# Kernel optimization log

Measured on AMD Instinct MI355X. Metric: run time of the kernel, lower is better.

The kernel has to match this reference:

```python
import jax, jax.numpy as jnp
import numpy as np

B, S, D, H = 2, 2048, 1024, 16
HD = D // H
EPS = 1e-5

def _ln(x, g, b):
    mu = jnp.mean(x, axis=-1, keepdims=True)
    var = jnp.var(x, axis=-1, keepdims=True)
    return (x - mu) * jax.lax.rsqrt(var + EPS) * g + b

def setup_inputs() -> dict:
    key = jax.random.key(0)
    ks = jax.random.split(key, 6)
    sc = lambda n: 1.0 / np.sqrt(n)
    return {
        "x": jax.random.normal(ks[0], (B, S, D), jnp.float32),
        "W_qkv": jax.random.normal(ks[1], (D, 3 * D), jnp.float32) * sc(D),
        "b_qkv": jnp.zeros((3 * D,), jnp.float32),
        "W_o": jax.random.normal(ks[2], (D, D), jnp.float32) * sc(D),
        "b_o": jnp.zeros((D,), jnp.float32),
        "W_fc": jax.random.normal(ks[3], (D, 4 * D), jnp.float32) * sc(D),
        "b_fc": jnp.zeros((4 * D,), jnp.float32),
        "W_pr": jax.random.normal(ks[4], (4 * D, D), jnp.float32) * sc(4 * D),
        "b_pr": jnp.zeros((D,), jnp.float32),
        "g1": jnp.ones((D,), jnp.float32),
        "beta1": jnp.zeros((D,), jnp.float32),
        "g2": jnp.ones((D,), jnp.float32),
        "beta2": jnp.zeros((D,), jnp.float32),
    }

def reference(x, W_qkv, b_qkv, W_o, b_o, W_fc, b_fc, W_pr, b_pr, g1, beta1, g2, beta2):
    # pre-norm attention
    h = _ln(x, g1, beta1)
    qkv = h @ W_qkv + b_qkv                      # [B,S,3D]
    q, k, v = jnp.split(qkv, 3, axis=-1)
    q = q.reshape(B, S, H, HD).transpose(0, 2, 1, 3)  # [B,H,S,hd]
    k = k.reshape(B, S, H, HD).transpose(0, 2, 1, 3)
    v = v.reshape(B, S, H, HD).transpose(0, 2, 1, 3)
    scores = jnp.einsum('bhqd,bhkd->bhqk', q, k) / np.sqrt(HD)
    causal = jnp.tril(jnp.ones((S, S), bool))
    scores = jnp.where(causal, scores, -jnp.inf)
    attn = jax.nn.softmax(scores, axis=-1)
    out = jnp.einsum('bhqk,bhkd->bhqd', attn, v)
    out = out.transpose(0, 2, 1, 3).reshape(B, S, D)
    x = x + out @ W_o + b_o
    # pre-norm MLP (exact erf GELU, matching torch F.gelu default)
    h2 = _ln(x, g2, beta2)
    h2 = jax.nn.gelu(h2 @ W_fc + b_fc, approximate=False)
    x = x + h2 @ W_pr + b_pr
    return x
```

## Files before the change

kernel.cpp:

```cpp
#include <hip/hip_runtime.h>
#include <cstdint>
#include <cstddef>

#define Bb 2
#define Ss 2048
#define Dd 1024
#define Hh 16

typedef __attribute__((ext_vector_type(8))) short short8;
typedef __attribute__((ext_vector_type(4))) short short4v;
typedef __attribute__((ext_vector_type(4))) float float4v;

__device__ inline short f2bf(float f) {
  unsigned u = __builtin_bit_cast(unsigned, f);
  u = (u + 0x7fffu + ((u >> 16) & 1u)) >> 16;
  return (short)u;
}

__device__ inline float bf2f(short s) {
  unsigned u = ((unsigned)(unsigned short)s) << 16;
  return __builtin_bit_cast(float, u);
}

__device__ inline void gl_lds16(const void* g, void* l) {
  __builtin_amdgcn_global_load_lds(
      (__attribute__((address_space(1))) void*)(void*)(g),
      (__attribute__((address_space(3))) void*)(l), 16, 0, 0);
}

#define MFMA(a, b, c) __builtin_amdgcn_mfma_f32_16x16x32_bf16((a), (b), (c), 0, 0, 0)

__device__ __forceinline__ void ln_row(const float* __restrict__ x,
                                       const float* __restrict__ g,
                                       const float* __restrict__ be,
                                       short* __restrict__ out, int row,
                                       float* red) {
  int tid = threadIdx.x;
  const float4* xr = (const float4*)(x + (size_t)row * Dd);
  float4 v = xr[tid];
  float s = v.x + v.y + v.z + v.w;
  float q = v.x * v.x + v.y * v.y + v.z * v.z + v.w * v.w;
#pragma unroll
  for (int off = 1; off < 64; off <<= 1) {
    s += __shfl_xor(s, off);
    q += __shfl_xor(q, off);
  }
  int w = tid >> 6;
  if ((tid & 63) == 0) { red[w] = s; red[4 + w] = q; }
  __syncthreads();
  s = red[0] + red[1] + red[2] + red[3];
  q = red[4] + red[5] + red[6] + red[7];
  float mu = s * (1.0f / Dd);
  float var = q * (1.0f / Dd) - mu * mu;
  float rstd = rsqrtf(var + 1e-5f);
  float4 gv = ((const float4*)g)[tid], bv = ((const float4*)be)[tid];
  short4v o;
  o.x = f2bf((v.x - mu) * rstd * gv.x + bv.x);
  o.y = f2bf((v.y - mu) * rstd * gv.y + bv.y);
  o.z = f2bf((v.z - mu) * rstd * gv.z + bv.z);
  o.w = f2bf((v.w - mu) * rstd * gv.w + bv.w);
  *(short4v*)(out + (size_t)row * Dd + tid * 4) = o;
}

__global__ __launch_bounds__(256) void prep_kernel(
    const float* __restrict__ W0, short* __restrict__ T0,
    const float* __restrict__ W1, short* __restrict__ T1,
    const float* __restrict__ W2, short* __restrict__ T2,
    const float* __restrict__ W3, short* __restrict__ T3,
    const float* __restrict__ x, const float* __restrict__ g1,
    const float* __restrict__ be1, short* __restrict__ h1) {
  __shared__ __align__(16) float t[32][33];
  int id = blockIdx.x;
  if (id >= 12288) {
    ln_row(x, g1, be1, h1, id - 12288, &t[0][0]);
    return;
  }
  const float* W; short* Wt; int N, K, tix;
  if (id < 3072)      { W = W0; Wt = T0; N = 3072; K = 1024; tix = id; }
  else if (id < 4096) { W = W1; Wt = T1; N = 1024; K = 1024; tix = id - 3072; }
  else if (id < 8192) { W = W2; Wt = T2; N = 4096; K = 1024; tix = id - 4096; }
  else                { W = W3; Wt = T3; N = 1024; K = 4096; tix = id - 8192; }
  int nx = N / 32;
  int n0 = (tix % nx) * 32, k0 = (tix / nx) * 32;
  int tx = threadIdx.x & 31, ty = threadIdx.x >> 5;
#pragma unroll
  for (int i = 0; i < 4; i++)
    t[ty + 8 * i][tx] = W[(size_t)(k0 + ty + 8 * i) * N + n0 + tx];
  __syncthreads();
#pragma unroll
  for (int i = 0; i < 4; i++)
    Wt[(size_t)(n0 + ty + 8 * i) * K + k0 + tx] = f2bf(t[tx][ty + 8 * i]);
}

__global__ __launch_bounds__(256) void reduce_ln_kernel(const float* __restrict__ x,
                                                        const float* __restrict__ bias,
                                                        const short* __restrict__ parts,
                                                        const float* __restrict__ g,
                                                        const float* __restrict__ be,
                                                        float* __restrict__ x1,
                                                        short* __restrict__ h2) {
  int row = blockIdx.x, tid = threadIdx.x;
  size_t base = (size_t)row * Dd + tid * 4;
  float4 v = *(const float4*)(x + base);
  float4 bv = ((const float4*)bias)[tid];
  v.x += bv.x; v.y += bv.y; v.z += bv.z; v.w += bv.w;
#pragma unroll
  for (int s = 0; s < 4; s++) {
    short4v p = *(const short4v*)(parts + (size_t)s * 4096 * Dd + base);
    v.x += bf2f(p.x); v.y += bf2f(p.y); v.z += bf2f(p.z); v.w += bf2f(p.w);
  }
  *(float4*)(x1 + base) = v;
  float s = v.x + v.y + v.z + v.w;
  float q = v.x * v.x + v.y * v.y + v.z * v.z + v.w * v.w;
#pragma unroll
  for (int off = 1; off < 64; off <<= 1) {
    s += __shfl_xor(s, off);
    q += __shfl_xor(q, off);
  }
  __shared__ float as_[4], aq_[4];
  int w = tid >> 6;
  if ((tid & 63) == 0) { as_[w] = s; aq_[w] = q; }
  __syncthreads();
  s = as_[0] + as_[1] + as_[2] + as_[3];
  q = aq_[0] + aq_[1] + aq_[2] + aq_[3];
  float mu = s * (1.0f / Dd);
  float var = q * (1.0f / Dd) - mu * mu;
  float rstd = rsqrtf(var + 1e-5f);
  float4 gv = ((const float4*)g)[tid], b2 = ((const float4*)be)[tid];
  short4v o;
  o.x = f2bf((v.x - mu) * rstd * gv.x + b2.x);
  o.y = f2bf((v.y - mu) * rstd * gv.y + b2.y);
  o.z = f2bf((v.z - mu) * rstd * gv.z + b2.z);
  o.w = f2bf((v.w - mu) * rstd * gv.w + b2.w);
  *(short4v*)(h2 + base) = o;
}

__global__ __launch_bounds__(256) void reduce_kernel(const float* __restrict__ src,
                                                     const float* __restrict__ bias,
                                                     const short* __restrict__ parts,
                                                     float* __restrict__ dst) {
  int row = blockIdx.x, tid = threadIdx.x;
  size_t base = (size_t)row * Dd + tid * 4;
  float4 v = *(const float4*)(src + base);
  float4 bv = ((const float4*)bias)[tid];
  v.x += bv.x; v.y += bv.y; v.z += bv.z; v.w += bv.w;
#pragma unroll
  for (int s = 0; s < 4; s++) {
    short4v p = *(const short4v*)(parts + (size_t)s * 4096 * Dd + base);
    v.x += bf2f(p.x); v.y += bf2f(p.y); v.z += bf2f(p.z); v.w += bf2f(p.w);
  }
  *(float4*)(dst + base) = v;
}

template <int MODE>
__device__ __forceinline__ void gemm256(const short* __restrict__ A,
                                        const short* __restrict__ Bt,
                                        const float* __restrict__ bias,
                                        void* __restrict__ outp,
                                        short* __restrict__ vtp,
                                        int M, int N, int K,
                                        int m0, int n0, int zp,
                                        int ks, int nt, char* smem) {
  const int tid = threadIdx.x;
  const int wid = tid >> 6, lane = tid & 63;
  const int wm = wid >> 2, wn = wid & 3;
  const int fr = lane & 15, g = lane >> 4;
  const int r0 = tid >> 3, sl = tid & 7;
  const int gcs = sl ^ (r0 & 7);
  const int lOff = r0 * 128 + sl * 16;

  const short* gA = A + (size_t)(m0 + r0) * K + ks + gcs * 8;
  const short* gB = Bt + (size_t)(n0 + r0) * K + ks + gcs * 8;

  auto stageA = [&](int t) {
    char* la = smem + (t & 1) * 65536 + lOff;
    const short* ga = gA + t * 64;
#pragma unroll
    for (int i = 0; i < 4; i++)
      gl_lds16(ga + (size_t)(64 * i) * K, la + i * 8192);
  };
  auto stageB = [&](int t) {
    char* lb = smem + (t & 1) * 65536 + 32768 + lOff;
    const short* gb = gB + t * 64;
#pragma unroll
    for (int i = 0; i < 4; i++)
      gl_lds16(gb + (size_t)(64 * i) * K, lb + i * 8192);
  };

  const int aoff0 = (g ^ (fr & 7)) * 16;
  const int aoff1 = ((g + 4) ^ (fr & 7)) * 16;
  const int arow = (wm * 128 + fr) * 128;
  const int brow = (wn * 64 + fr) * 128;

  float4v acc[8][4] = {};
  short8 a[4][2], b[4][2];

  stageA(0);
  stageB(0);
  if (nt > 1) {
    stageA(1);
    asm volatile("s_waitcnt vmcnt(4)" ::: "memory");
  } else {
    asm volatile("s_waitcnt vmcnt(0)" ::: "memory");
  }
  __builtin_amdgcn_s_barrier();

  for (int t = 0; t < nt; t++) {
    char* lA = smem + (t & 1) * 65536;
    char* lB = lA + 32768;
#pragma unroll
    for (int i = 0; i < 4; i++) {
      a[i][0] = *(const short8*)(lA + arow + i * 2048 + aoff0);
      a[i][1] = *(const short8*)(lA + arow + i * 2048 + aoff1);
    }
    if (t + 1 < nt) stageB(t + 1);
#pragma unroll
    for (int j = 0; j < 2; j++) {
      b[j][0] = *(const short8*)(lB + brow + j * 2048 + aoff0);
      b[j][1] = *(const short8*)(lB + brow + j * 2048 + aoff1);
    }
    __builtin_amdgcn_s_barrier();
    asm volatile("s_waitcnt lgkmcnt(0)" ::: "memory");
    __builtin_amdgcn_s_setprio(1);
#pragma unroll
    for (int i = 0; i < 4; i++)
#pragma unroll
      for (int j = 0; j < 2; j++) {
        acc[i][j] = MFMA(a[i][0], b[j][0], acc[i][j]);
        acc[i][j] = MFMA(a[i][1], b[j][1], acc[i][j]);
      }
    __builtin_amdgcn_s_setprio(0);
    __builtin_amdgcn_s_barrier();
#pragma unroll
    for (int j = 2; j < 4; j++) {
      b[j][0] = *(const short8*)(lB + brow + j * 2048 + aoff0);
      b[j][1] = *(const short8*)(lB + brow + j * 2048 + aoff1);
    }
    __builtin_amdgcn_s_barrier();
    asm volatile("s_waitcnt lgkmcnt(0)" ::: "memory");
    __builtin_amdgcn_s_setprio(1);
#pragma unroll
    for (int i = 0; i < 4; i++)
#pragma unroll
      for (int j = 2; j < 4; j++) {
        acc[i][j] = MFMA(a[i][0], b[j][0], acc[i][j]);
        acc[i][j] = MFMA(a[i][1], b[j][1], acc[i][j]);
      }
    __builtin_amdgcn_s_setprio(0);
    __builtin_amdgcn_s_barrier();
#pragma unroll
    for (int i = 0; i < 4; i++) {
      a[i][0] = *(const short8*)(lA + arow + 8192 + i * 2048 + aoff0);
      a[i][1] = *(const short8*)(lA + arow + 8192 + i * 2048 + aoff1);
    }
    __builtin_amdgcn_s_barrier();
    asm volatile("s_waitcnt lgkmcnt(0)" ::: "memory");
    __builtin_amdgcn_s_setprio(1);
#pragma unroll
    for (int i = 0; i < 4; i++)
#pragma unroll
      for (int j = 2; j < 4; j++) {
        acc[4 + i][j] = MFMA(a[i][0], b[j][0], acc[4 + i][j]);
        acc[4 + i][j] = MFMA(a[i][1], b[j][1], acc[4 + i][j]);
      }
    __builtin_amdgcn_s_setprio(0);
    __builtin_amdgcn_s_barrier();
    if (t + 2 < nt) stageA(t + 2);
    __builtin_amdgcn_s_setprio(1);
#pragma unroll
    for (int i = 0; i < 4; i++)
#pragma unroll
      for (int j = 0; j < 2; j++) {
        acc[4 + i][j] = MFMA(a[i][0], b[j][0], acc[4 + i][j]);
        acc[4 + i][j] = MFMA(a[i][1], b[j][1], acc[4 + i][j]);
      }
    __builtin_amdgcn_s_setprio(0);
    if (t + 1 < nt) {
      if (t + 2 < nt)
        asm volatile("s_waitcnt vmcnt(4)" ::: "memory");
      else
        asm volatile("s_waitcnt vmcnt(0)" ::: "memory");
      __builtin_amdgcn_s_barrier();
    }
  }

  const int crow = g * 4;
#pragma unroll
  for (int i = 0; i < 8; i++) {
#pragma unroll
    for (int j = 0; j < 4; j++) {
      int col = n0 + wn * 64 + j * 16 + fr;
      float bcol = (MODE == 3) ? 0.f : bias[col];
      short sh[4];
#pragma unroll
      for (int r = 0; r < 4; r++) {
        int row = m0 + wm * 128 + i * 16 + crow + r;
        float v = acc[i][j][r] + bcol;
        if (MODE == 4) {
          sh[r] = f2bf(v);
          ((short*)outp)[(size_t)row * N + col] = sh[r];
        } else if (MODE == 2) {
          float y = 0.79788456f * (v + 0.044715f * v * v * v);
          float e = __builtin_amdgcn_exp2f(y * 2.885390082f);
          float th = 1.0f - 2.0f * __builtin_amdgcn_rcpf(e + 1.0f);
          v = 0.5f * v * (1.0f + th);
          ((short*)outp)[(size_t)row * N + col] = f2bf(v);
        } else {
          short* pp = (short*)outp + (size_t)zp * M * N;
          pp[(size_t)row * N + col] = f2bf(v);
        }
      }
      if (MODE == 4 && col >= 2048) {
        int hd = col - 2048;
        int rbase = m0 + wm * 128 + i * 16 + crow;
        int bq = rbase >> 11, sb = rbase & 2047;
        int bh = bq * 16 + (hd >> 6), d = hd & 63;
        short4v pk;
        pk.x = sh[0]; pk.y = sh[1]; pk.z = sh[2]; pk.w = sh[3];
        *(short4v*)(vtp + (size_t)(bh * 64 + d) * Ss + sb) = pk;
      }
    }
  }
}

__global__ __launch_bounds__(512, 2) void k_gemm_qkv(const short* __restrict__ A,
                                                     const short* __restrict__ Bt,
                                                     const float* __restrict__ bias,
                                                     short* __restrict__ o,
                                                     short* __restrict__ Vt) {
  extern __shared__ char smem[];
  int xcd = blockIdx.x & 7, u = blockIdx.x >> 3;
  int m0 = ((xcd >> 1) * 4 + u / 6) * 256;
  int n0 = ((xcd & 1) * 6 + u % 6) * 256;
  gemm256<4>(A, Bt, bias, o, Vt, 4096, 3072, 1024, m0, n0, 0, 0, 16, smem);
}

__global__ __launch_bounds__(512, 2) void k_gemm_fc(const short* __restrict__ A,
                                                    const short* __restrict__ Bt,
                                                    const float* __restrict__ bias,
                                                    short* __restrict__ o) {
  extern __shared__ char smem[];
  int xcd = blockIdx.x & 7, u = blockIdx.x >> 3;
  int m0 = ((xcd >> 1) * 4 + (u >> 3)) * 256;
  int n0 = ((xcd & 1) * 8 + (u & 7)) * 256;
  gemm256<2>(A, Bt, bias, o, nullptr, 4096, 4096, 1024, m0, n0, 0, 0, 16, smem);
}

__global__ __launch_bounds__(512, 2) void k_gemm_wo(const short* __restrict__ A,
                                                    const short* __restrict__ Bt,
                                                    short* __restrict__ parts) {
  extern __shared__ char smem[];
  int xcd = blockIdx.x & 7, u = blockIdx.x >> 3;
  int z = u >> 3;
  int m0 = (xcd * 2 + ((u >> 2) & 1)) * 256;
  int n0 = (u & 3) * 256;
  gemm256<3>(A, Bt, nullptr, parts, nullptr, 4096, 1024, 1024, m0, n0, z,
             z * 256, 4, smem);
}

__global__ __launch_bounds__(512, 2) void k_gemm_pr(const short* __restrict__ A,
                                                    const short* __restrict__ Bt,
                                                    short* __restrict__ parts) {
  extern __shared__ char smem[];
  int xcd = blockIdx.x & 7, u = blockIdx.x >> 3;
  int z = u >> 3;
  int m0 = (xcd * 2 + ((u >> 2) & 1)) * 256;
  int n0 = (u & 3) * 256;
  gemm256<3>(A, Bt, nullptr, parts, nullptr, 4096, 1024, 4096, m0, n0, z,
             z * 1024, 16, smem);
}

__global__ __launch_bounds__(256) void flash_kernel(const short* __restrict__ qkv,
                                                    const short* __restrict__ Vt,
                                                    short* __restrict__ att) {
  __shared__ __align__(16) short Ks[4096];
  __shared__ __align__(16) short Vs[4096];
  __shared__ __align__(16) short P[4][16 * 72];
  const int w = threadIdx.x >> 6, lane = threadIdx.x & 63;
  const int qb = 31 - (blockIdx.x >> 5);
  const int bh = blockIdx.x & 31;
  const int b = bh >> 4, h = bh & 15;
  const int qbase = qb * 64 + w * 16;
  const int q = lane & 15;
  const int g = lane >> 4;
  const int fk = g * 8;
  short* Pw = &P[w][0];

  const int L0 = w * 64 + lane, L1 = L0 + 256;
  const int r0 = L0 >> 3, c0 = (L0 & 7) ^ (r0 & 7);
  const int r1 = L1 >> 3, c1 = (L1 & 7) ^ (r1 & 7);
  const short* kg0 = qkv + (size_t)(b * Ss + r0) * 3072 + 1024 + h * 64 + c0 * 8;
  const short* kg1 = qkv + (size_t)(b * Ss + r1) * 3072 + 1024 + h * 64 + c1 * 8;
  const short* vg0 = Vt + (size_t)(bh * 64 + r0) * Ss + c0 * 8;
  const short* vg1 = Vt + (size_t)(bh * 64 + r1) * Ss + c1 * 8;

  short8 qf[2];
  {
    const short* qrow = qkv + (size_t)(b * Ss + qbase + q) * 3072 + h * 64;
    qf[0] = *(const short8*)(qrow + fk);
    qf[1] = *(const short8*)(qrow + 32 + fk);
  }
  float4v o[4] = {};
  float l_i = 0.f;
  const float sc = 0.125f * 1.44269504088896f;
  const int nkt = qb + 1;

  gl_lds16(kg0, Ks + L0 * 8);
  gl_lds16(kg1, Ks + L1 * 8);
  gl_lds16(vg0, Vs + L0 * 8);
  gl_lds16(vg1, Vs + L1 * 8);

  for (int kt = 0; kt < nkt; kt++) {
    const int kbase = kt * 64;
    __syncthreads();

    short8 kf[4][2], vf[4][2];
#pragma unroll
    for (int t = 0; t < 4; t++) {
      const int row = 16 * t + q;
      const int sw = (g ^ (row & 7)) * 8;
      kf[t][0] = *(const short8*)(Ks + row * 64 + sw);
      kf[t][1] = *(const short8*)(Ks + row * 64 + (sw ^ 32));
      vf[t][0] = *(const short8*)(Vs + row * 64 + sw);
      vf[t][1] = *(const short8*)(Vs + row * 64 + (sw ^ 32));
    }
    __syncthreads();
    if (kt + 1 < nkt) {
      const size_t nb = (size_t)(kbase + 64);
      gl_lds16(kg0 + nb * 3072, Ks + L0 * 8);
      gl_lds16(kg1 + nb * 3072, Ks + L1 * 8);
      gl_lds16(vg0 + nb, Vs + L0 * 8);
      gl_lds16(vg1 + nb, Vs + L1 * 8);
    }

    float4v s[4] = {};
#pragma unroll
    for (int t = 0; t < 4; t++) {
      s[t] = MFMA(kf[t][0], qf[0], s[t]);
      s[t] = MFMA(kf[t][1], qf[1], s[t]);
    }
    const bool maskt = (kbase + 63 > qbase);
    const int qlim = qbase + q - kbase;
    float p[4][4];
    float rs = 0.f;
#pragma unroll
    for (int t = 0; t < 4; t++) {
#pragma unroll
      for (int r = 0; r < 4; r++) {
        float v = s[t][r] * sc;
        if (maskt && (16 * t + 4 * g + r > qlim)) v = -3.0e38f;
        float e = __builtin_amdgcn_exp2f(v);
        p[t][r] = e;
        rs += e;
      }
    }
    rs += __shfl_xor(rs, 16);
    rs += __shfl_xor(rs, 32);
    l_i += rs;
#pragma unroll
    for (int t = 0; t < 4; t++) {
      unsigned lo = (unsigned)(unsigned short)f2bf(p[t][0]) |
                    ((unsigned)(unsigned short)f2bf(p[t][1]) << 16);
      unsigned hi = (unsigned)(unsigned short)f2bf(p[t][2]) |
                    ((unsigned)(unsigned short)f2bf(p[t][3]) << 16);
      uint2 u; u.x = lo; u.y = hi;
      *(uint2*)(Pw + q * 72 + 16 * t + 4 * g) = u;
    }
    asm volatile("s_waitcnt lgkmcnt(0)" ::: "memory");
    short8 pb0 = *(const short8*)(Pw + q * 72 + fk);
    short8 pb1 = *(const short8*)(Pw + q * 72 + 32 + fk);
#pragma unroll
    for (int t = 0; t < 4; t++) {
      o[t] = MFMA(vf[t][0], pb0, o[t]);
      o[t] = MFMA(vf[t][1], pb1, o[t]);
    }
  }
  const float inv = 1.0f / l_i;
  const int orow = b * Ss + qbase + q;
#pragma unroll
  for (int t = 0; t < 4; t++) {
    short4v ov;
    ov.x = f2bf(o[t][0] * inv);
    ov.y = f2bf(o[t][1] * inv);
    ov.z = f2bf(o[t][2] * inv);
    ov.w = f2bf(o[t][3] * inv);
    *(short4v*)(att + (size_t)orow * Dd + h * 64 + 16 * t + 4 * g) = ov;
  }
}

extern "C" void kernel_launch(void* const* d_in, const int* in_sizes, int n_in,
                              void* d_out, int out_size, void* d_ws, size_t ws_size,
                              hipStream_t stream) {
  const float* x    = (const float*)d_in[0];
  const float* Wqkv = (const float*)d_in[1];
  const float* bqkv = (const float*)d_in[2];
  const float* Wo   = (const float*)d_in[3];
  const float* bo   = (const float*)d_in[4];
  const float* Wfc  = (const float*)d_in[5];
  const float* bfc  = (const float*)d_in[6];
  const float* Wpr  = (const float*)d_in[7];
  const float* bpr  = (const float*)d_in[8];
  const float* g1   = (const float*)d_in[9];
  const float* be1  = (const float*)d_in[10];
  const float* g2   = (const float*)d_in[11];
  const float* be2  = (const float*)d_in[12];

  char* ws = (char*)d_ws;
  const size_t MB = 1024 * 1024;
  short* h1     = (short*)(ws + 0);
  short* qkvb   = (short*)(ws + 8 * MB);
  short* partWo = (short*)(ws + 0);
  short* partPr = (short*)(ws + 0);
  short* Vt     = (short*)(ws + 32 * MB);
  short* att    = (short*)(ws + 40 * MB);
  float* x1     = (float*)(ws + 48 * MB);
  short* h2     = (short*)(ws + 64 * MB);
  short* geluo  = (short*)(ws + 72 * MB);
  short* WtQkv  = (short*)(ws + 104 * MB);
  short* WtO    = (short*)(ws + 110 * MB);
  short* WtFc   = (short*)(ws + 112 * MB);
  short* WtPr   = (short*)(ws + 120 * MB);

  prep_kernel<<<16384, 256, 0, stream>>>(Wqkv, WtQkv, Wo, WtO, Wfc, WtFc,
                                         Wpr, WtPr, x, g1, be1, h1);
  k_gemm_qkv<<<192, 512, 131072, stream>>>(h1, WtQkv, bqkv, qkvb, Vt);
  flash_kernel<<<1024, 256, 0, stream>>>(qkvb, Vt, att);
  k_gemm_wo<<<256, 512, 131072, stream>>>(att, WtO, partWo);
  reduce_ln_kernel<<<4096, 256, 0, stream>>>(x, bo, partWo, g2, be2, x1, h2);
  k_gemm_fc<<<256, 512, 131072, stream>>>(h2, WtFc, bfc, geluo);
  k_gemm_pr<<<256, 512, 131072, stream>>>(geluo, WtPr, partPr);
  reduce_kernel<<<4096, 256, 0, stream>>>(x1, bpr, partPr, (float*)d_out);
}
```

Before: 311.5 us.

## Restructure GEMM pipeline into half-tile staged loads interleaved with MFMA phases

Replaces the per-tile double-buffered staging of the 256x256 GEMM with a finer-grained schedule. Each tile's A and B loads are split into halves, and each half is issued between the four MFMA sub-phases. The loop is unrolled by two over a ping-pong buffer, with an explicit prologue and epilogue. The aim is to spread global-to-LDS traffic across compute phases and keep more loads in flight, hiding memory latency better. The new schedule assumes an even tile count of at least 4, and the B row mapping per wave is changed, which adds correctness risk for other shapes.

```diff
diff --git a/kernel.cpp b/kernel.cpp
--- a/kernel.cpp
+++ b/kernel.cpp
@@ -29,6 +29,9 @@
 }
 
 #define MFMA(a, b, c) __builtin_amdgcn_mfma_f32_16x16x32_bf16((a), (b), (c), 0, 0, 0)
+#define BAR() __builtin_amdgcn_s_barrier()
+#define LGKM0() asm volatile("s_waitcnt lgkmcnt(0)" ::: "memory")
+#define VMC(n) asm volatile("s_waitcnt vmcnt(" #n ")" ::: "memory")
 
 __device__ __forceinline__ void ln_row(const float* __restrict__ x,
                                        const float* __restrict__ g,
@@ -165,27 +168,26 @@
   const int wid = tid >> 6, lane = tid & 63;
   const int wm = wid >> 2, wn = wid & 3;
   const int fr = lane & 15, g = lane >> 4;
-  const int r0 = tid >> 3, sl = tid & 7;
-  const int gcs = sl ^ (r0 & 7);
-  const int lOff = r0 * 128 + sl * 16;
-
-  const short* gA = A + (size_t)(m0 + r0) * K + ks + gcs * 8;
-  const short* gB = Bt + (size_t)(n0 + r0) * K + ks + gcs * 8;
-
-  auto stageA = [&](int t) {
-    char* la = smem + (t & 1) * 65536 + lOff;
-    const short* ga = gA + t * 64;
-#pragma unroll
-    for (int i = 0; i < 4; i++)
-      gl_lds16(ga + (size_t)(64 * i) * K, la + i * 8192);
+  const int rA = tid >> 3, sl = tid & 7;
+  const int gcs = sl ^ (rA & 7);
+  const int lOff = rA * 128 + sl * 16;
+  const int rB = (wid >> 2) * 64 + (wid & 3) * 8 + (lane >> 3);
+  const int lOffB = rB * 128 + sl * 16;
+
+  const short* gA = A + (size_t)(m0 + rA) * K + ks + gcs * 8;
+  const short* gB = Bt + (size_t)(n0 + rB) * K + ks + gcs * 8;
+
+  auto sA = [&](int bo, int roff, int t) {
+    gl_lds16(gA + (size_t)roff * K + (size_t)t * 64, smem + bo + roff * 128 + lOff);
   };
-  auto stageB = [&](int t) {
-    char* lb = smem + (t & 1) * 65536 + 32768 + lOff;
-    const short* gb = gB + t * 64;
-#pragma unroll
-    for (int i = 0; i < 4; i++)
-      gl_lds16(gb + (size_t)(64 * i) * K, lb + i * 8192);
+  auto sB = [&](int bo, int roff, int t) {
+    gl_lds16(gB + (size_t)roff * K + (size_t)t * 64,
+             smem + bo + 32768 + roff * 128 + lOffB);
   };
+  auto AH0 = [&](int bo, int t) { sA(bo, 0, t); sA(bo, 128, t); };
+  auto AH1 = [&](int bo, int t) { sA(bo, 64, t); sA(bo, 192, t); };
+  auto BH0 = [&](int bo, int t) { sB(bo, 0, t); sB(bo, 128, t); };
+  auto BH1 = [&](int bo, int t) { sB(bo, 32, t); sB(bo, 160, t); };
 
   const int aoff0 = (g ^ (fr & 7)) * 16;
   const int aoff1 = ((g + 4) ^ (fr & 7)) * 16;
@@ -195,94 +197,77 @@
   float4v acc[8][4] = {};
   short8 a[4][2], b[4][2];
 
-  stageA(0);
-  stageB(0);
-  if (nt > 1) {
-    stageA(1);
-    asm volatile("s_waitcnt vmcnt(4)" ::: "memory");
-  } else {
-    asm volatile("s_waitcnt vmcnt(0)" ::: "memory");
-  }
-  __builtin_amdgcn_s_barrier();
-
-  for (int t = 0; t < nt; t++) {
-    char* lA = smem + (t & 1) * 65536;
-    char* lB = lA + 32768;
+  auto RA = [&](int bo, int half) {
+    const char* p = smem + bo + arow + half * 8192;
 #pragma unroll
     for (int i = 0; i < 4; i++) {
-      a[i][0] = *(const short8*)(lA + arow + i * 2048 + aoff0);
-      a[i][1] = *(const short8*)(lA + arow + i * 2048 + aoff1);
-    }
-    if (t + 1 < nt) stageB(t + 1);
+      a[i][0] = *(const short8*)(p + i * 2048 + aoff0);
+      a[i][1] = *(const short8*)(p + i * 2048 + aoff1);
+    }
+  };
+  auto RB = [&](int bo, int jh) {
+    const char* p = smem + bo + 32768 + brow + jh * 4096;
 #pragma unroll
     for (int j = 0; j < 2; j++) {
-      b[j][0] = *(const short8*)(lB + brow + j * 2048 + aoff0);
-      b[j][1] = *(const short8*)(lB + brow + j * 2048 + aoff1);
-    }
-    __builtin_amdgcn_s_barrier();
-    asm volatile("s_waitcnt lgkmcnt(0)" ::: "memory");
+      b[2 * jh + j][0] = *(const short8*)(p + j * 2048 + aoff0);
+      b[2 * jh + j][1] = *(const short8*)(p + j * 2048 + aoff1);
+    }
+  };
+  auto MM = [&](int qi, int qj) {
     __builtin_amdgcn_s_setprio(1);
 #pragma unroll
     for (int i = 0; i < 4; i++)
 #pragma unroll
       for (int j = 0; j < 2; j++) {
-        acc[i][j] = MFMA(a[i][0], b[j][0], acc[i][j]);
-        acc[i][j] = MFMA(a[i][1], b[j][1], acc[i][j]);
+        const int jj = 2 * qj + j;
+        acc[4 * qi + i][jj] = MFMA(a[i][0], b[jj][0], acc[4 * qi + i][jj]);
+        acc[4 * qi + i][jj] = MFMA(a[i][1], b[jj][1], acc[4 * qi + i][jj]);
       }
     __builtin_amdgcn_s_setprio(0);
-    __builtin_amdgcn_s_barrier();
-#pragma unroll
-    for (int j = 2; j < 4; j++) {
-      b[j][0] = *(const short8*)(lB + brow + j * 2048 + aoff0);
-      b[j][1] = *(const short8*)(lB + brow + j * 2048 + aoff1);
-    }
-    __builtin_amdgcn_s_barrier();
-    asm volatile("s_waitcnt lgkmcnt(0)" ::: "memory");
-    __builtin_amdgcn_s_setprio(1);
-#pragma unroll
-    for (int i = 0; i < 4; i++)
-#pragma unroll
-      for (int j = 2; j < 4; j++) {
-        acc[i][j] = MFMA(a[i][0], b[j][0], acc[i][j]);
-        acc[i][j] = MFMA(a[i][1], b[j][1], acc[i][j]);
-      }
-    __builtin_amdgcn_s_setprio(0);
-    __builtin_amdgcn_s_barrier();
-#pragma unroll
-    for (int i = 0; i < 4; i++) {
-      a[i][0] = *(const short8*)(lA + arow + 8192 + i * 2048 + aoff0);
-      a[i][1] = *(const short8*)(lA + arow + 8192 + i * 2048 + aoff1);
-    }
-    __builtin_amdgcn_s_barrier();
-    asm volatile("s_waitcnt lgkmcnt(0)" ::: "memory");
-    __builtin_amdgcn_s_setprio(1);
-#pragma unroll
-    for (int i = 0; i < 4; i++)
-#pragma unroll
-      for (int j = 2; j < 4; j++) {
-        acc[4 + i][j] = MFMA(a[i][0], b[j][0], acc[4 + i][j]);
-        acc[4 + i][j] = MFMA(a[i][1], b[j][1], acc[4 + i][j]);
-      }
-    __builtin_amdgcn_s_setprio(0);
-    __builtin_amdgcn_s_barrier();
-    if (t + 2 < nt) stageA(t + 2);
-    __builtin_amdgcn_s_setprio(1);
-#pragma unroll
-    for (int i = 0; i < 4; i++)
-#pragma unroll
-      for (int j = 0; j < 2; j++) {
-        acc[4 + i][j] = MFMA(a[i][0], b[j][0], acc[4 + i][j]);
-        acc[4 + i][j] = MFMA(a[i][1], b[j][1], acc[4 + i][j]);
-      }
-    __builtin_amdgcn_s_setprio(0);
-    if (t + 1 < nt) {
-      if (t + 2 < nt)
-        asm volatile("s_waitcnt vmcnt(4)" ::: "memory");
-      else
-        asm volatile("s_waitcnt vmcnt(0)" ::: "memory");
-      __builtin_amdgcn_s_barrier();
-    }
-  }
+  };
+
+  AH0(0, 0); BH0(0, 0); BH1(0, 0); AH1(0, 0);
+  AH0(65536, 1); BH0(65536, 1); BH1(65536, 1);
+  VMC(6);
+  BAR();
+
+  const int nit = nt / 2 - 1;
+  for (int it = 0; it < nit; ++it) {
+    const int t1 = 2 * it + 1, t2 = 2 * it + 2, t3 = 2 * it + 3;
+    RA(0, 0); RB(0, 0); AH1(65536, t1);
+    BAR(); LGKM0(); MM(0, 0); BAR();
+    RB(0, 1); AH0(0, t2);
+    BAR(); LGKM0(); MM(0, 1); BAR();
+    RA(0, 1); BH0(0, t2);
+    BAR(); LGKM0(); MM(1, 1); BAR();
+    BH1(0, t2);
+    MM(1, 0);
+    VMC(6); BAR();
+    RA(65536, 0); RB(65536, 0); AH1(0, t2);
+    BAR(); LGKM0(); MM(0, 0); BAR();
+    RB(65536, 1); AH0(65536, t3);
+    BAR(); LGKM0(); MM(0, 1); BAR();
+    RA(65536, 1); BH0(65536, t3);
+    BAR(); LGKM0(); MM(1, 1); BAR();
+    BH1(65536, t3);
+    MM(1, 0);
+    VMC(6); BAR();
+  }
+  RA(0, 0); RB(0, 0); AH1(65536, nt - 1);
+  BAR(); LGKM0(); MM(0, 0); BAR();
+  RB(0, 1);
+  BAR(); LGKM0(); MM(0, 1); BAR();
+  RA(0, 1);
+  BAR(); LGKM0(); MM(1, 1); BAR();
+  MM(1, 0);
+  VMC(0); BAR();
+  RA(65536, 0); RB(65536, 0);
+  BAR(); LGKM0(); MM(0, 0); BAR();
+  RB(65536, 1);
+  BAR(); LGKM0(); MM(0, 1); BAR();
+  RA(65536, 1);
+  BAR(); LGKM0(); MM(1, 1); BAR();
+  MM(1, 0);
 
   const int crow = g * 4;
 #pragma unroll
```

After: 303.6 us. 1.03x faster.
